# Performance work log

Measured on AMD Instinct MI355X. Metric: run time of the kernel, lower is better.

Reference implementation:

```python
import jax, jax.numpy as jnp
import numpy as np

BATCH = 8192
MAX_PIECES = 32
NNZ = BATCH * MAX_PIECES
FT_OUT = 512
N_FEATURES = 768


def setup_inputs() -> dict:
    key = jax.random.key(0)
    ks = jax.random.split(key, 8)
    # COO indices: row 0 = batch index (each position contributes MAX_PIECES features),
    # row 1 = feature index in [0, 768)
    batch_ids = jnp.repeat(jnp.arange(BATCH, dtype=jnp.int64), MAX_PIECES)
    stm_feat = jax.random.randint(ks[0], (NNZ,), 0, N_FEATURES, dtype=jnp.int64)
    nstm_feat = jax.random.randint(ks[1], (NNZ,), 0, N_FEATURES, dtype=jnp.int64)
    stm_indices = jnp.stack([batch_ids, stm_feat])   # [2, nnz]
    nstm_indices = jnp.stack([batch_ids, nstm_feat])  # [2, nnz]
    values = jnp.ones((NNZ,), dtype=jnp.float32)      # binary features
    # Linear(768, FT_OUT): store weight transposed as [768, FT_OUT]
    ft_w = jax.random.normal(ks[2], (N_FEATURES, FT_OUT), dtype=jnp.float32) * (1.0 / np.sqrt(N_FEATURES))
    ft_b = jax.random.normal(ks[3], (FT_OUT,), dtype=jnp.float32) * 0.01
    # Linear(2*FT_OUT, 1): stored as [2*FT_OUT, 1]
    out_w = jax.random.normal(ks[4], (2 * FT_OUT, 1), dtype=jnp.float32) * (1.0 / np.sqrt(2 * FT_OUT))
    out_b = jax.random.normal(ks[5], (1,), dtype=jnp.float32) * 0.01
    return {
        "stm_indices": stm_indices,
        "nstm_indices": nstm_indices,
        "values": values,
        "ft_w": ft_w,
        "ft_b": ft_b,
        "out_w": out_w,
        "out_b": out_b,
        "batch_size": BATCH,
    }


def reference(stm_indices, nstm_indices, values, ft_w, ft_b, out_w, out_b, batch_size):
    def feature_transform(indices):
        # sparse @ W^T + b  ==  gather rows of W^T by feature id, scale by value,
        # segment-sum into batch rows. rows: [nnz, FT_OUT]
        rows = ft_w[indices[1]] * values[:, None]
        acc = jax.ops.segment_sum(rows, indices[0], num_segments=batch_size)
        return acc + ft_b

    stm_ft = feature_transform(stm_indices)    # [B, FT_OUT]
    nstm_ft = feature_transform(nstm_indices)  # [B, FT_OUT]
    hidden = jnp.clip(jnp.concatenate([stm_ft, nstm_ft], axis=1), 0.0, 1.0)
    return jax.nn.sigmoid(hidden @ out_w + out_b)  # [B, 1]
```

## Files before the change

### kernel.cpp

```cpp
#include <hip/hip_runtime.h>
#include <math.h>

#define MAX_PIECES 32
#define FT_OUT 512
#define NFEAT 768
#define QSCALE 512.0f
#define INV_QSCALE (1.0f / 512.0f)

typedef unsigned int u32x2 __attribute__((ext_vector_type(2)));

__global__ __launch_bounds__(256) void cvt_i8(
    const float* __restrict__ ft_w, unsigned int* __restrict__ qtab, int n)
{
    const int i = (blockIdx.x * 256 + threadIdx.x) * 4;
    if (i >= n) return;
    const float4 f = *(const float4*)(ft_w + i);
    const float vf[4] = {f.x, f.y, f.z, f.w};
    unsigned int packed = 0;
    #pragma unroll
    for (int j = 0; j < 4; ++j) {
        float q = rintf(vf[j] * QSCALE);
        q = fminf(fmaxf(q, -127.f), 127.f);
        const unsigned int b = (unsigned int)(int)(q + 128.f);
        packed |= (b & 0xffu) << (8 * j);
    }
    qtab[i >> 2] = packed;
}

__global__ __launch_bounds__(256) void nnue_fwd(
    const int*   __restrict__ stm_idx,
    const int*   __restrict__ nstm_idx,
    const float* __restrict__ values,
    const unsigned char* __restrict__ qtab,
    const float* __restrict__ ft_b,
    const float* __restrict__ out_w,
    const float* __restrict__ out_b,
    float*       __restrict__ out,
    int nnz)
{
    const int t    = threadIdx.x;
    const int g    = t >> 6;
    const int lane = t & 63;
    const int side = g & 1;
    const int row  = blockIdx.x * 2 + (g >> 1);

    __shared__ float s_red[4];

    const int* __restrict__ src = side ? nstm_idx : stm_idx;
    const int meta  = row * MAX_PIECES + (lane & 31);
    const int myidx = src[nnz + meta];
    const int myvali = __float_as_int(values[meta]);

    const int colb = lane * 8;

    float acc[8];
    #pragma unroll
    for (int j = 0; j < 8; ++j) acc[j] = 0.f;
    float vsum = 0.f;

    #pragma unroll
    for (int i = 0; i < MAX_PIECES; ++i) {
        const int   f = __builtin_amdgcn_readlane(myidx, i);
        const float v = __int_as_float(__builtin_amdgcn_readlane(myvali, i));
        vsum += v;
        const u32x2* rowp = (const u32x2*)(qtab + f * FT_OUT);
        const u32x2 u = __builtin_nontemporal_load(rowp + lane);
        acc[0] = fmaf((float)( u[0]        & 0xffu), v, acc[0]);
        acc[1] = fmaf((float)((u[0] >>  8) & 0xffu), v, acc[1]);
        acc[2] = fmaf((float)((u[0] >> 16) & 0xffu), v, acc[2]);
        acc[3] = fmaf((float)( u[0] >> 24         ), v, acc[3]);
        acc[4] = fmaf((float)( u[1]        & 0xffu), v, acc[4]);
        acc[5] = fmaf((float)((u[1] >>  8) & 0xffu), v, acc[5]);
        acc[6] = fmaf((float)((u[1] >> 16) & 0xffu), v, acc[6]);
        acc[7] = fmaf((float)( u[1] >> 24         ), v, acc[7]);
    }

    const float qoff = 128.f * vsum;

    const float4 b0 = *(const float4*)(ft_b + colb);
    const float4 b1 = *(const float4*)(ft_b + colb + 4);
    const float bb[8] = {b0.x, b0.y, b0.z, b0.w, b1.x, b1.y, b1.z, b1.w};
    const float4 w0 = *(const float4*)(out_w + side * FT_OUT + colb);
    const float4 w1 = *(const float4*)(out_w + side * FT_OUT + colb + 4);
    const float ww[8] = {w0.x, w0.y, w0.z, w0.w, w1.x, w1.y, w1.z, w1.w};

    float p = 0.f;
    #pragma unroll
    for (int j = 0; j < 8; ++j) {
        const float h = fminf(fmaxf(fmaf(acc[j] - qoff, INV_QSCALE, bb[j]), 0.f), 1.f);
        p = fmaf(h, ww[j], p);
    }

    #pragma unroll
    for (int off = 32; off > 0; off >>= 1)
        p += __shfl_down(p, off, 64);
    if (lane == 0) s_red[g] = p;
    __syncthreads();

    if (t < 2) {
        const float s = s_red[2 * t] + s_red[2 * t + 1] + out_b[0];
        out[blockIdx.x * 2 + t] = 1.f / (1.f + expf(-s));
    }
}

extern "C" void kernel_launch(void* const* d_in, const int* in_sizes, int n_in,
                              void* d_out, int out_size, void* d_ws, size_t ws_size,
                              hipStream_t stream) {
    const int*   stm_idx  = (const int*)d_in[0];
    const int*   nstm_idx = (const int*)d_in[1];
    const float* values   = (const float*)d_in[2];
    const float* ft_w     = (const float*)d_in[3];
    const float* ft_b     = (const float*)d_in[4];
    const float* out_w    = (const float*)d_in[5];
    const float* out_b    = (const float*)d_in[6];
    float*       out      = (float*)d_out;

    const int nnz = in_sizes[0] / 2;
    const int B   = out_size;
    const int nw  = NFEAT * FT_OUT;

    unsigned int* qtab = (unsigned int*)d_ws;

    cvt_i8<<<(nw / 4 + 255) / 256, 256, 0, stream>>>(ft_w, qtab, nw);
    nnue_fwd<<<B / 2, 256, 0, stream>>>(stm_idx, nstm_idx, values,
                                        (const unsigned char*)qtab,
                                        ft_b, out_w, out_b, out, nnz);
}
```

Baseline: 89.03 us.

## Split wave into two half-waves each loading 16-byte row chunks for alternating pieces

Each wavefront now splits into two halves that process even and odd pieces. Each lane loads 16 bytes (one 128-bit load) covering 16 output columns instead of 8 bytes. This halves the number of gather iterations and widens each memory transaction. The halves' accumulators are then combined with a cross-half xor shuffle. In exchange it doubles the accumulator registers, adds 16 shuffles for the merge, and does redundant work in the epilogue, which is corrected by scaling by 0.5.

After: 91.76 us. 1.03x slower.

```diff
diff --git a/kernel.cpp b/kernel.cpp
--- a/kernel.cpp
+++ b/kernel.cpp
@@ -7,7 +7,7 @@
 #define QSCALE 512.0f
 #define INV_QSCALE (1.0f / 512.0f)
 
-typedef unsigned int u32x2 __attribute__((ext_vector_type(2)));
+typedef unsigned int u32x4 __attribute__((ext_vector_type(4)));
 
 __global__ __launch_bounds__(256) void cvt_i8(
     const float* __restrict__ ft_w, unsigned int* __restrict__ qtab, int n)
@@ -21,8 +21,7 @@
     for (int j = 0; j < 4; ++j) {
         float q = rintf(vf[j] * QSCALE);
         q = fminf(fmaxf(q, -127.f), 127.f);
-        const unsigned int b = (unsigned int)(int)(q + 128.f);
-        packed |= (b & 0xffu) << (8 * j);
+        packed |= ((unsigned int)(int)(q + 128.f) & 0xffu) << (8 * j);
     }
     qtab[i >> 2] = packed;
 }
@@ -41,60 +40,68 @@
     const int t    = threadIdx.x;
     const int g    = t >> 6;
     const int lane = t & 63;
+    const int half = lane >> 5;
+    const int l31  = lane & 31;
     const int side = g & 1;
     const int row  = blockIdx.x * 2 + (g >> 1);
 
     __shared__ float s_red[4];
 
     const int* __restrict__ src = side ? nstm_idx : stm_idx;
-    const int meta  = row * MAX_PIECES + (lane & 31);
-    const int myidx = src[nnz + meta];
+    const int meta   = row * MAX_PIECES + l31;
+    const int myidx  = src[nnz + meta];
     const int myvali = __float_as_int(values[meta]);
 
-    const int colb = lane * 8;
-
-    float acc[8];
+    float acc[16];
     #pragma unroll
-    for (int j = 0; j < 8; ++j) acc[j] = 0.f;
+    for (int j = 0; j < 16; ++j) acc[j] = 0.f;
     float vsum = 0.f;
 
+    const unsigned char* __restrict__ qbase = qtab + (l31 << 4);
+
     #pragma unroll
-    for (int i = 0; i < MAX_PIECES; ++i) {
-        const int   f = __builtin_amdgcn_readlane(myidx, i);
-        const float v = __int_as_float(__builtin_amdgcn_readlane(myvali, i));
+    for (int i = 0; i < 16; ++i) {
+        const int   p = 2 * i + half;
+        const int   f = __shfl(myidx, p, 64);
+        const float v = __int_as_float(__shfl(myvali, p, 64));
         vsum += v;
-        const u32x2* rowp = (const u32x2*)(qtab + f * FT_OUT);
-        const u32x2 u = __builtin_nontemporal_load(rowp + lane);
-        acc[0] = fmaf((float)( u[0]        & 0xffu), v, acc[0]);
-        acc[1] = fmaf((float)((u[0] >>  8) & 0xffu), v, acc[1]);
-        acc[2] = fmaf((float)((u[0] >> 16) & 0xffu), v, acc[2]);
-        acc[3] = fmaf((float)( u[0] >> 24         ), v, acc[3]);
-        acc[4] = fmaf((float)( u[1]        & 0xffu), v, acc[4]);
-        acc[5] = fmaf((float)((u[1] >>  8) & 0xffu), v, acc[5]);
-        acc[6] = fmaf((float)((u[1] >> 16) & 0xffu), v, acc[6]);
-        acc[7] = fmaf((float)( u[1] >> 24         ), v, acc[7]);
-    }
-
-    const float qoff = 128.f * vsum;
-
-    const float4 b0 = *(const float4*)(ft_b + colb);
-    const float4 b1 = *(const float4*)(ft_b + colb + 4);
-    const float bb[8] = {b0.x, b0.y, b0.z, b0.w, b1.x, b1.y, b1.z, b1.w};
-    const float4 w0 = *(const float4*)(out_w + side * FT_OUT + colb);
-    const float4 w1 = *(const float4*)(out_w + side * FT_OUT + colb + 4);
-    const float ww[8] = {w0.x, w0.y, w0.z, w0.w, w1.x, w1.y, w1.z, w1.w};
-
-    float p = 0.f;
-    #pragma unroll
-    for (int j = 0; j < 8; ++j) {
-        const float h = fminf(fmaxf(fmaf(acc[j] - qoff, INV_QSCALE, bb[j]), 0.f), 1.f);
-        p = fmaf(h, ww[j], p);
+        const u32x4 u = __builtin_nontemporal_load(
+            (const u32x4*)(qbase + ((long)f << 9)));
+        #pragma unroll
+        for (int k = 0; k < 4; ++k) {
+            const unsigned int w = u[k];
+            acc[4 * k + 0] = fmaf((float)( w        & 0xffu), v, acc[4 * k + 0]);
+            acc[4 * k + 1] = fmaf((float)((w >>  8) & 0xffu), v, acc[4 * k + 1]);
+            acc[4 * k + 2] = fmaf((float)((w >> 16) & 0xffu), v, acc[4 * k + 2]);
+            acc[4 * k + 3] = fmaf((float)( w >> 24         ), v, acc[4 * k + 3]);
+        }
     }
 
     #pragma unroll
-    for (int off = 32; off > 0; off >>= 1)
-        p += __shfl_down(p, off, 64);
-    if (lane == 0) s_red[g] = p;
+    for (int j = 0; j < 16; ++j) acc[j] += __shfl_xor(acc[j], 32, 64);
+    vsum += __shfl_xor(vsum, 32, 64);
+    const float qoff = 128.f * vsum;
+
+    const int colb = l31 * 16;
+    float pacc = 0.f;
+    #pragma unroll
+    for (int q = 0; q < 4; ++q) {
+        const float4 bb = *(const float4*)(ft_b + colb + 4 * q);
+        const float4 ww = *(const float4*)(out_w + side * FT_OUT + colb + 4 * q);
+        const float bv[4] = {bb.x, bb.y, bb.z, bb.w};
+        const float wv[4] = {ww.x, ww.y, ww.z, ww.w};
+        #pragma unroll
+        for (int j = 0; j < 4; ++j) {
+            const float h = fminf(fmaxf(
+                fmaf(acc[4 * q + j] - qoff, INV_QSCALE, bv[j]), 0.f), 1.f);
+            pacc = fmaf(h, wv[j], pacc);
+        }
+    }
+
+    #pragma unroll
+    for (int off = 1; off < 64; off <<= 1)
+        pacc += __shfl_xor(pacc, off, 64);
+    if (lane == 0) s_red[g] = 0.5f * pacc;
     __syncthreads();
 
     if (t < 2) {
```

## Stream int8 weight rows into LDS via async global_load_lds with 4-deep pipeline

Applied to the files above, without the earlier changes.

Replaces direct per-piece global row loads with async global-to-LDS copies of 16 bytes per lane, two feature rows per chunk, into a 4-slot ring buffer per wavefront. Explicit vmcnt waits and scheduling barriers keep several chunks in flight while earlier chunks are decoded and accumulated. The value sum is now computed up front with a butterfly reduction. The change adds LDS traffic, hand-coded waitcnt encodings and scheduling barriers that constrain the compiler.

New measurement: 89.06 us. No clear change (+0.0%).

```diff
diff --git a/kernel.cpp b/kernel.cpp
--- a/kernel.cpp
+++ b/kernel.cpp
@@ -1,5 +1,6 @@
 #include <hip/hip_runtime.h>
 #include <math.h>
+#include <stdint.h>
 
 #define MAX_PIECES 32
 #define FT_OUT 512
@@ -21,10 +22,28 @@
     for (int j = 0; j < 4; ++j) {
         float q = rintf(vf[j] * QSCALE);
         q = fminf(fmaxf(q, -127.f), 127.f);
-        const unsigned int b = (unsigned int)(int)(q + 128.f);
-        packed |= (b & 0xffu) << (8 * j);
+        packed |= ((unsigned int)(int)(q + 128.f) & 0xffu) << (8 * j);
     }
     qtab[i >> 2] = packed;
+}
+
+__device__ __forceinline__ void async_load16(const unsigned char* g, unsigned char* lds)
+{
+    __builtin_amdgcn_global_load_lds(
+        (const __attribute__((address_space(1))) unsigned int*)(uintptr_t)g,
+        (__attribute__((address_space(3))) unsigned int*)(uintptr_t)lds,
+        16, 0, 0);
+}
+
+__device__ __forceinline__ void wait_vm(int n)
+{
+    switch (n) {
+        case 0: __builtin_amdgcn_s_waitcnt(0x0f70); break;
+        case 1: __builtin_amdgcn_s_waitcnt(0x0f71); break;
+        case 2: __builtin_amdgcn_s_waitcnt(0x0f72); break;
+        default: __builtin_amdgcn_s_waitcnt(0x0f73); break;
+    }
+    __builtin_amdgcn_sched_barrier(0);
 }
 
 __global__ __launch_bounds__(256) void nnue_fwd(
@@ -41,42 +60,67 @@
     const int t    = threadIdx.x;
     const int g    = t >> 6;
     const int lane = t & 63;
+    const int l31  = lane & 31;
+    const int half = lane >> 5;
     const int side = g & 1;
     const int row  = blockIdx.x * 2 + (g >> 1);
 
+    __shared__ __align__(16) unsigned char s_buf[4][4][1024];
     __shared__ float s_red[4];
 
     const int* __restrict__ src = side ? nstm_idx : stm_idx;
-    const int meta  = row * MAX_PIECES + (lane & 31);
-    const int myidx = src[nnz + meta];
+    const int meta   = row * MAX_PIECES + l31;
+    const int myidx  = src[nnz + meta];
     const int myvali = __float_as_int(values[meta]);
 
-    const int colb = lane * 8;
+    float vs = __int_as_float(myvali);
+    #pragma unroll
+    for (int off = 1; off < 64; off <<= 1) vs += __shfl_xor(vs, off, 64);
+    const float qoff = 128.f * (0.5f * vs);
+
+    unsigned char* mybuf = &s_buf[g][0][0];
+    const int laneoff = l31 * 16;
+
+    #define ISSUE(c)                                                          \
+        do {                                                                  \
+            const int fe = __builtin_amdgcn_readlane(myidx, 2 * (c));         \
+            const int fo = __builtin_amdgcn_readlane(myidx, 2 * (c) + 1);     \
+            const int roff = (half ? fo : fe) * FT_OUT;                       \
+            async_load16(qtab + roff + laneoff, mybuf + (((c) & 3) << 10));   \
+        } while (0)
 
     float acc[8];
     #pragma unroll
     for (int j = 0; j < 8; ++j) acc[j] = 0.f;
-    float vsum = 0.f;
+
+    ISSUE(0); ISSUE(1); ISSUE(2); ISSUE(3);
 
     #pragma unroll
-    for (int i = 0; i < MAX_PIECES; ++i) {
-        const int   f = __builtin_amdgcn_readlane(myidx, i);
-        const float v = __int_as_float(__builtin_amdgcn_readlane(myvali, i));
-        vsum += v;
-        const u32x2* rowp = (const u32x2*)(qtab + f * FT_OUT);
-        const u32x2 u = __builtin_nontemporal_load(rowp + lane);
-        acc[0] = fmaf((float)( u[0]        & 0xffu), v, acc[0]);
-        acc[1] = fmaf((float)((u[0] >>  8) & 0xffu), v, acc[1]);
-        acc[2] = fmaf((float)((u[0] >> 16) & 0xffu), v, acc[2]);
-        acc[3] = fmaf((float)( u[0] >> 24         ), v, acc[3]);
-        acc[4] = fmaf((float)( u[1]        & 0xffu), v, acc[4]);
-        acc[5] = fmaf((float)((u[1] >>  8) & 0xffu), v, acc[5]);
-        acc[6] = fmaf((float)((u[1] >> 16) & 0xffu), v, acc[6]);
-        acc[7] = fmaf((float)( u[1] >> 24         ), v, acc[7]);
+    for (int c = 0; c < 16; ++c) {
+        wait_vm(c < 13 ? 3 : 15 - c);
+        const unsigned char* cb = mybuf + ((c & 3) << 10);
+        const u32x2 e = *(const u32x2*)(cb + lane * 8);
+        const u32x2 o = *(const u32x2*)(cb + 512 + lane * 8);
+        const float ve = __int_as_float(__builtin_amdgcn_readlane(myvali, 2 * c));
+        const float vo = __int_as_float(__builtin_amdgcn_readlane(myvali, 2 * c + 1));
+        #pragma unroll
+        for (int k = 0; k < 2; ++k) {
+            const unsigned int we = e[k], wo = o[k];
+            acc[4*k+0] = fmaf((float)( we        & 0xffu), ve, acc[4*k+0]);
+            acc[4*k+1] = fmaf((float)((we >>  8) & 0xffu), ve, acc[4*k+1]);
+            acc[4*k+2] = fmaf((float)((we >> 16) & 0xffu), ve, acc[4*k+2]);
+            acc[4*k+3] = fmaf((float)( we >> 24         ), ve, acc[4*k+3]);
+            acc[4*k+0] = fmaf((float)( wo        & 0xffu), vo, acc[4*k+0]);
+            acc[4*k+1] = fmaf((float)((wo >>  8) & 0xffu), vo, acc[4*k+1]);
+            acc[4*k+2] = fmaf((float)((wo >> 16) & 0xffu), vo, acc[4*k+2]);
+            acc[4*k+3] = fmaf((float)( wo >> 24         ), vo, acc[4*k+3]);
+        }
+        __builtin_amdgcn_sched_barrier(0);
+        if (c + 4 < 16) ISSUE(c + 4);
     }
+    #undef ISSUE
 
-    const float qoff = 128.f * vsum;
-
+    const int colb = lane * 8;
     const float4 b0 = *(const float4*)(ft_b + colb);
     const float4 b1 = *(const float4*)(ft_b + colb + 4);
     const float bb[8] = {b0.x, b0.y, b0.z, b0.w, b1.x, b1.y, b1.z, b1.w};
```
